# Kernel tuning notes

Hardware: AMD Instinct MI355X
Metric: run time of the kernel (lower is better)

Reference implementation:

```python
import jax, jax.numpy as jnp
import numpy as np

B, L, C, H, W = 4, 32, 16, 64, 64


def setup_inputs() -> dict:
    key = jax.random.key(0)
    k1, k2 = jax.random.split(key)
    # small flows so warps stay mostly local (realistic optical-flow magnitudes)
    flows = jax.random.normal(k1, (B, L, 2, H, W), dtype=jnp.float32) * 0.1
    images = jax.random.normal(k2, (B, L, C, H, W), dtype=jnp.float32)
    return {"flows": flows, "images": images}


def _wrap(x):
    # wrap_coord: map into [-1, 1) periodically (jnp.mod with positive divisor is non-negative)
    return jnp.mod(x + 1.0, 2.0) - 1.0


def _bilinear(images, ix, iy):
    # images: [B, K, C, H, W]; ix, iy: [B, K, H, W] pixel-space coords
    Bb, K, Cc, Hh, Ww = images.shape
    x0 = jnp.floor(ix).astype(jnp.int32)
    y0 = jnp.floor(iy).astype(jnp.int32)
    x1 = x0 + 1
    y1 = y0 + 1
    wx1 = ix - x0.astype(ix.dtype)
    wy1 = iy - y0.astype(iy.dtype)
    wx0 = 1.0 - wx1
    wy0 = 1.0 - wy1
    flat = images.reshape(Bb, K, Cc, Hh * Ww)

    def gat(xi, yi):
        valid = ((xi >= 0) & (xi < Ww) & (yi >= 0) & (yi < Hh)).astype(images.dtype)
        idx = (jnp.clip(yi, 0, Hh - 1) * Ww + jnp.clip(xi, 0, Ww - 1)).reshape(Bb, K, 1, Hh * Ww)
        v = jnp.take_along_axis(flat, idx, axis=3).reshape(Bb, K, Cc, Hh, Ww)
        return v * valid[:, :, None]  # zero padding outside image

    return ((wx0 * wy0)[:, :, None] * gat(x0, y0)
            + (wx1 * wy0)[:, :, None] * gat(x1, y0)
            + (wx0 * wy1)[:, :, None] * gat(x0, y1)
            + (wx1 * wy1)[:, :, None] * gat(x1, y1))


def _forward(flows, images):
    Bb, Ll, Cc, Hh, Ww = images.shape
    # cumulative flow, computed in fp32 then cast back (matches torch.cumsum(...).to(dtype))
    cum = jnp.cumsum(flows.astype(jnp.float32), axis=1).astype(flows.dtype)  # [B,L,2,H,W]
    bx = (jnp.arange(Ww, dtype=jnp.float32) + 0.5) * (2.0 / Ww) - 1.0
    by = (jnp.arange(Hh, dtype=jnp.float32) + 0.5) * (2.0 / Hh) - 1.0
    base_x = jnp.broadcast_to(bx[None, :], (Hh, Ww))
    base_y = jnp.broadcast_to(by[:, None], (Hh, Ww))
    # mask[t, k] = 1 iff k <= t (causal accumulation over past frames)
    mask = jnp.tril(jnp.ones((Ll, Ll), dtype=images.dtype))

    def step(carry, inp):
        cum_t, mrow = inp  # cum_t: [B,2,H,W], mrow: [L]
        rel = cum_t[:, None] - cum  # [B,L,2,H,W] = flow_t - flow_k
        gx = _wrap(base_x + rel[:, :, 0])
        gy = _wrap(base_y + rel[:, :, 1])
        ix = (gx + 1.0) * 0.5 * Ww - 0.5
        iy = (gy + 1.0) * 0.5 * Hh - 0.5
        warped = _bilinear(images, ix, iy)  # [B,L,C,H,W]
        out_t = jnp.einsum('blchw,l->bchw', warped, mrow)
        return carry, out_t

    _, ys = jax.lax.scan(step, None, (jnp.moveaxis(cum, 1, 0), mask))
    return jnp.moveaxis(ys, 0, 1)  # [B,L,C,H,W]


def reference(flows, images):
    return _forward(flows, images)
```

## Files before the change

### kernel.cpp

```cpp
#include <hip/hip_runtime.h>


constexpr int BN = 4, LN = 32, CN = 16, HWn = 4096;
constexpr int FRAME = CN * HWn;
constexpr size_t TIMG_BYTES = (size_t)BN * LN * HWn * CN * 2;
constexpr size_t CUM_BYTES  = (size_t)BN * LN * HWn * 2 * 4;

__global__ __launch_bounds__(256) void prep_timg(
        const float* __restrict__ img, float4* __restrict__ timg) {
    const int bi = blockIdx.x, tile = bi & 15, f = bi >> 4;
    const int p = (tile << 8) + threadIdx.x;
    const float* src = img + (size_t)f * FRAME + p;
#pragma unroll
    for (int g = 0; g < 2; ++g) {
        union { float4 f4; _Float16 h[8]; } cell;
#pragma unroll
        for (int j = 0; j < 8; ++j)
            cell.h[j] = (_Float16)src[(g * 8 + j) * HWn];
        timg[((size_t)f * 2 + g) * HWn + p] = cell.f4;
    }
}

__global__ __launch_bounds__(256) void prep_cum(
        const float* __restrict__ flows, float2* __restrict__ cum) {
    const int b = blockIdx.x >> 4;
    const int p = ((blockIdx.x & 15) << 8) + threadIdx.x;
    const float* fl = flows + (size_t)b * (LN * 2 * HWn) + p;
    float cx = 0.f, cy = 0.f;
    for (int l = 0; l < LN; ++l) {
        cx += fl[(2 * l) * HWn];
        cy += fl[(2 * l + 1) * HWn];
        cum[(size_t)(b * LN + l) * HWn + p] = make_float2(cx, cy);
    }
}

__device__ __forceinline__ void px_step(const float4* __restrict__ fr,
                                        float2 ct, float2 ck,
                                        float bx, float by,
                                        float* __restrict__ acc) {
    float vx = (bx + (ct.x - ck.x)) + 1.0f;
    float vy = (by + (ct.y - ck.y)) + 1.0f;
    float mx = vx - 2.0f * floorf(vx * 0.5f);
    float my = vy - 2.0f * floorf(vy * 0.5f);
    float ix = ((mx - 1.0f) + 1.0f) * 32.0f - 0.5f;
    float iy = ((my - 1.0f) + 1.0f) * 32.0f - 0.5f;
    float xf = floorf(ix), yf = floorf(iy);
    int x0 = (int)xf, y0 = (int)yf;
    float wx1 = ix - xf, wy1 = iy - yf;
    float wx0 = 1.0f - wx1, wy0 = 1.0f - wy1;
    wx0 = (x0 >= 0) ? wx0 : 0.0f;
    wx1 = (x0 <= 62) ? wx1 : 0.0f;
    wy0 = (y0 >= 0) ? wy0 : 0.0f;
    wy1 = (y0 <= 62) ? wy1 : 0.0f;
    const int x0c = max(x0, 0), y0c = max(y0, 0);
    const int x1c = min(x0 + 1, 63), y1c = min(y0 + 1, 63);
    const float w00 = wx0 * wy0, w10 = wx1 * wy0;
    const float w01 = wx0 * wy1, w11 = wx1 * wy1;
    union { float4 f4; _Float16 h[8]; } g00, g10, g01, g11;
    g00.f4 = fr[(y0c << 6) + x0c];
    g10.f4 = fr[(y0c << 6) + x1c];
    g01.f4 = fr[(y1c << 6) + x0c];
    g11.f4 = fr[(y1c << 6) + x1c];
#pragma unroll
    for (int c = 0; c < 8; ++c)
        acc[c] += ((w00 * (float)g00.h[c] + w10 * (float)g10.h[c])
                   + w01 * (float)g01.h[c]) + w11 * (float)g11.h[c];
}

__global__ __launch_bounds__(1024, 4) void gsps_lds(
        const float2* __restrict__ cum,
        const char* __restrict__ timg,
        float* __restrict__ out) {
    extern __shared__ char smem[];
    const int bid = blockIdx.x;
    const int xs  = bid & 7;
    const int b   = xs >> 1;
    const int pxh = xs & 1;
    const int seq = bid >> 3;
    const int pair = seq & 15;
    const int chh  = seq >> 4;
    const int tid = threadIdx.x;
    const int t1 = 31 - pair;
    const int t2 = pair;

    const int px0 = (pxh << 11) + tid;
    const int px1 = px0 + 1024;
    const float bx0 = ((float)(px0 & 63) + 0.5f) * 0.03125f - 1.0f;
    const float by0 = ((float)(px0 >> 6) + 0.5f) * 0.03125f - 1.0f;
    const float bx1 = ((float)(px1 & 63) + 0.5f) * 0.03125f - 1.0f;
    const float by1 = ((float)(px1 >> 6) + 0.5f) * 0.03125f - 1.0f;

    const float2* cb = cum + (size_t)b * (LN * HWn);
    const size_t chunk0 = (((size_t)b * LN * 2) + chh) << 16;
    const unsigned wbase = (unsigned)(tid & ~63) << 4;

#define STAGE(KK, BUF) do {                                                   \
    const char* gsrc = timg + chunk0 + ((size_t)(KK) << 17);                  \
    _Pragma("unroll")                                                         \
    for (int j = 0; j < 4; ++j) {                                             \
        __builtin_amdgcn_global_load_lds(                                     \
            (const __attribute__((address_space(1))) void*)                  \
                (gsrc + j * 16384 + tid * 16),                                \
            (__attribute__((address_space(3))) void*)                        \
                (smem + ((BUF) << 16) + wbase + j * 16384),                   \
            16, 0, 0);                                                        \
    }                                                                         \
} while (0)

    float acc0[8] = {0}, acc1[8] = {0};
    float2 ct0 = make_float2(0.f, 0.f), ct1 = ct0;
    float2 ckp0 = cb[px0], ckp1 = cb[px1];

    STAGE(0, 0);

    for (int i = 0; i < 33; ++i) {
        const bool ph2 = (i > t1);
        const int k = ph2 ? (i - t1 - 1) : i;
        const int t = ph2 ? t2 : t1;

        __syncthreads();
        if (i < 32) {
            const int kn = (i + 1 > t1) ? (i - t1) : (i + 1);
            STAGE(kn, (i + 1) & 1);
        }

        const float2 ck0 = ckp0, ck1 = ckp1;
        if (i < 32) {
            const int kn = (i + 1 > t1) ? (i - t1) : (i + 1);
            ckp0 = cb[kn * HWn + px0];
            ckp1 = cb[kn * HWn + px1];
        }
        if (k == 0) {
            ct0 = cb[t * HWn + px0];
            ct1 = cb[t * HWn + px1];
#pragma unroll
            for (int c = 0; c < 8; ++c) { acc0[c] = 0.f; acc1[c] = 0.f; }
        }
        const float4* fr = (const float4*)(smem + ((i & 1) << 16));
        px_step(fr, ct0, ck0, bx0, by0, acc0);
        px_step(fr, ct1, ck1, bx1, by1, acc1);

        if (k == t) {
            float* op = out + ((size_t)(b * LN + t) * CN + chh * 8) * HWn;
#pragma unroll
            for (int c = 0; c < 8; ++c) {
                op[c * HWn + px0] = acc0[c];
                op[c * HWn + px1] = acc1[c];
            }
        }
    }
#undef STAGE
}

__global__ __launch_bounds__(256) void gsps_slow(
        const float* __restrict__ flows,
        const float* __restrict__ img,
        float* __restrict__ out) {
    const int bi = blockIdx.x;
    const int tile = bi & 15;
    const int rest = bi >> 4;
    const int t = 31 - (rest & 31);
    const int b = rest >> 5;
    const int p = (tile << 8) + threadIdx.x;
    const int h = p >> 6, w = p & 63;
    const float base_x = ((float)w + 0.5f) * 0.03125f - 1.0f;
    const float base_y = ((float)h + 0.5f) * 0.03125f - 1.0f;
    const float* fl = flows + (size_t)b * (LN * 2 * HWn) + p;

    float ctx = 0.f, cty = 0.f;
    for (int j = 0; j <= t; ++j) { ctx += fl[(2*j)*HWn]; cty += fl[(2*j+1)*HWn]; }

    float acc[16];
#pragma unroll
    for (int c = 0; c < 16; ++c) acc[c] = 0.f;

    float ckx = 0.f, cky = 0.f;
    for (int k = 0; k <= t; ++k) {
        ckx += fl[(2*k)*HWn]; cky += fl[(2*k+1)*HWn];
        float vx = (base_x + (ctx - ckx)) + 1.0f;
        float vy = (base_y + (cty - cky)) + 1.0f;
        float mx = vx - 2.0f * floorf(vx * 0.5f);
        float my = vy - 2.0f * floorf(vy * 0.5f);
        const float ix = ((mx - 1.0f) + 1.0f) * 32.0f - 0.5f;
        const float iy = ((my - 1.0f) + 1.0f) * 32.0f - 0.5f;
        const float x0f = floorf(ix), y0f = floorf(iy);
        const int x0 = (int)x0f, y0 = (int)y0f;
        const float wx1 = ix - x0f, wy1 = iy - y0f;
        const float wx0 = 1.0f - wx1, wy0 = 1.0f - wy1;
        const int x1 = x0 + 1, y1 = y0 + 1;
        const float fx0 = (x0 >= 0) ? 1.0f : 0.0f;
        const float fx1 = (x1 <= 63) ? 1.0f : 0.0f;
        const float fy0 = (y0 >= 0) ? 1.0f : 0.0f;
        const float fy1 = (y1 <= 63) ? 1.0f : 0.0f;
        const int x0c = (x0 < 0) ? 0 : x0, x1c = (x1 > 63) ? 63 : x1;
        const int y0c = (y0 < 0) ? 0 : y0, y1c = (y1 > 63) ? 63 : y1;
        const float w00 = (wx0*wy0)*(fx0*fy0), w10 = (wx1*wy0)*(fx1*fy0);
        const float w01 = (wx0*wy1)*(fx0*fy1), w11 = (wx1*wy1)*(fx1*fy1);
        const float* frm = img + (size_t)(b * LN + k) * FRAME;
        const int i00 = (y0c<<6)+x0c, i10 = (y0c<<6)+x1c;
        const int i01 = (y1c<<6)+x0c, i11 = (y1c<<6)+x1c;
#pragma unroll
        for (int c = 0; c < 16; ++c) {
            const float* pl = frm + c * HWn;
            acc[c] += ((w00*pl[i00] + w10*pl[i10]) + w01*pl[i01]) + w11*pl[i11];
        }
    }
    float* op = out + (size_t)(b * LN + t) * FRAME + p;
#pragma unroll
    for (int c = 0; c < 16; ++c) op[c * HWn] = acc[c];
}

extern "C" void kernel_launch(void* const* d_in, const int* in_sizes, int n_in,
                              void* d_out, int out_size, void* d_ws, size_t ws_size,
                              hipStream_t stream) {
    const float* flows  = (const float*)d_in[0];
    const float* images = (const float*)d_in[1];
    float* out = (float*)d_out;

    bool fast = (ws_size >= TIMG_BYTES + CUM_BYTES);
    if (fast) {
        hipError_t e = hipFuncSetAttribute(
            reinterpret_cast<const void*>(&gsps_lds),
            hipFuncAttributeMaxDynamicSharedMemorySize, 131072);
        if (e != hipSuccess) fast = false;
    }
    if (fast) {
        float4* timg = (float4*)d_ws;
        float2* cumw = (float2*)((char*)d_ws + TIMG_BYTES);
        prep_timg<<<BN * LN * 16, 256, 0, stream>>>(images, timg);
        prep_cum<<<BN * 16, 256, 0, stream>>>(flows, cumw);
        gsps_lds<<<256, 1024, 131072, stream>>>(cumw, (const char*)timg, out);
    } else {
        gsps_slow<<<BN * LN * 16, 256, 0, stream>>>(flows, images, out);
    }
}
```

Measured before the change: 89.77 us.

## Single-buffer LDS stage with smaller blocks and more workgroups

```diff
diff --git a/kernel.cpp b/kernel.cpp
--- a/kernel.cpp
+++ b/kernel.cpp
@@ -42,8 +42,8 @@
     float vy = (by + (ct.y - ck.y)) + 1.0f;
     float mx = vx - 2.0f * floorf(vx * 0.5f);
     float my = vy - 2.0f * floorf(vy * 0.5f);
-    float ix = ((mx - 1.0f) + 1.0f) * 32.0f - 0.5f;
-    float iy = ((my - 1.0f) + 1.0f) * 32.0f - 0.5f;
+    float ix = mx * 32.0f - 0.5f;
+    float iy = my * 32.0f - 0.5f;
     float xf = floorf(ix), yf = floorf(iy);
     int x0 = (int)xf, y0 = (int)yf;
     float wx1 = ix - xf, wy1 = iy - yf;
@@ -57,34 +57,33 @@
     const float w00 = wx0 * wy0, w10 = wx1 * wy0;
     const float w01 = wx0 * wy1, w11 = wx1 * wy1;
     union { float4 f4; _Float16 h[8]; } g00, g10, g01, g11;
-    g00.f4 = fr[(y0c << 6) + x0c];
-    g10.f4 = fr[(y0c << 6) + x1c];
-    g01.f4 = fr[(y1c << 6) + x0c];
-    g11.f4 = fr[(y1c << 6) + x1c];
+    const int r0 = (y0c << 6), r1 = (y1c << 6);
+    g00.f4 = fr[r0 + x0c];
+    g10.f4 = fr[r0 + x1c];
+    g01.f4 = fr[r1 + x0c];
+    g11.f4 = fr[r1 + x1c];
 #pragma unroll
     for (int c = 0; c < 8; ++c)
         acc[c] += ((w00 * (float)g00.h[c] + w10 * (float)g10.h[c])
                    + w01 * (float)g01.h[c]) + w11 * (float)g11.h[c];
 }
 
-__global__ __launch_bounds__(1024, 4) void gsps_lds(
+__global__ __launch_bounds__(512, 4) void gsps_lds(
         const float2* __restrict__ cum,
         const char* __restrict__ timg,
         float* __restrict__ out) {
     extern __shared__ char smem[];
     const int bid = blockIdx.x;
-    const int xs  = bid & 7;
-    const int b   = xs >> 1;
-    const int pxh = xs & 1;
-    const int seq = bid >> 3;
-    const int pair = seq & 15;
-    const int chh  = seq >> 4;
-    const int tid = threadIdx.x;
+    const int pxq  = ((bid & 1) << 1) | ((bid >> 3) & 1);
+    const int b    = (bid >> 1) & 3;
+    const int pair = (bid >> 4) & 15;
+    const int chh  = bid >> 8;
+    const int tid  = threadIdx.x;
     const int t1 = 31 - pair;
     const int t2 = pair;
 
-    const int px0 = (pxh << 11) + tid;
-    const int px1 = px0 + 1024;
+    const int px0 = (pxq << 10) + tid;
+    const int px1 = px0 + 512;
     const float bx0 = ((float)(px0 & 63) + 0.5f) * 0.03125f - 1.0f;
     const float by0 = ((float)(px0 >> 6) + 0.5f) * 0.03125f - 1.0f;
     const float bx1 = ((float)(px1 & 63) + 0.5f) * 0.03125f - 1.0f;
@@ -94,15 +93,15 @@
     const size_t chunk0 = (((size_t)b * LN * 2) + chh) << 16;
     const unsigned wbase = (unsigned)(tid & ~63) << 4;
 
-#define STAGE(KK, BUF) do {                                                   \
+#define STAGE(KK) do {                                                        \
     const char* gsrc = timg + chunk0 + ((size_t)(KK) << 17);                  \
     _Pragma("unroll")                                                         \
-    for (int j = 0; j < 4; ++j) {                                             \
+    for (int j = 0; j < 8; ++j) {                                             \
         __builtin_amdgcn_global_load_lds(                                     \
             (const __attribute__((address_space(1))) void*)                  \
-                (gsrc + j * 16384 + tid * 16),                                \
+                (gsrc + j * 8192 + tid * 16),                                 \
             (__attribute__((address_space(3))) void*)                        \
-                (smem + ((BUF) << 16) + wbase + j * 16384),                   \
+                (smem + wbase + j * 8192),                                    \
             16, 0, 0);                                                        \
     }                                                                         \
 } while (0)
@@ -110,8 +109,6 @@
     float acc0[8] = {0}, acc1[8] = {0};
     float2 ct0 = make_float2(0.f, 0.f), ct1 = ct0;
     float2 ckp0 = cb[px0], ckp1 = cb[px1];
-
-    STAGE(0, 0);
 
     for (int i = 0; i < 33; ++i) {
         const bool ph2 = (i > t1);
@@ -119,10 +116,8 @@
         const int t = ph2 ? t2 : t1;
 
         __syncthreads();
-        if (i < 32) {
-            const int kn = (i + 1 > t1) ? (i - t1) : (i + 1);
-            STAGE(kn, (i + 1) & 1);
-        }
+        STAGE(i == 0 ? 0 : k);
+        __syncthreads();
 
         const float2 ck0 = ckp0, ck1 = ckp1;
         if (i < 32) {
@@ -136,7 +131,7 @@
 #pragma unroll
             for (int c = 0; c < 8; ++c) { acc0[c] = 0.f; acc1[c] = 0.f; }
         }
-        const float4* fr = (const float4*)(smem + ((i & 1) << 16));
+        const float4* fr = (const float4*)smem;
         px_step(fr, ct0, ck0, bx0, by0, acc0);
         px_step(fr, ct1, ck1, bx1, by1, acc1);
 
@@ -221,7 +216,7 @@
     if (fast) {
         hipError_t e = hipFuncSetAttribute(
             reinterpret_cast<const void*>(&gsps_lds),
-            hipFuncAttributeMaxDynamicSharedMemorySize, 131072);
+            hipFuncAttributeMaxDynamicSharedMemorySize, 65536);
         if (e != hipSuccess) fast = false;
     }
     if (fast) {
@@ -229,7 +224,7 @@
         float2* cumw = (float2*)((char*)d_ws + TIMG_BYTES);
         prep_timg<<<BN * LN * 16, 256, 0, stream>>>(images, timg);
         prep_cum<<<BN * 16, 256, 0, stream>>>(flows, cumw);
-        gsps_lds<<<256, 1024, 131072, stream>>>(cumw, (const char*)timg, out);
+        gsps_lds<<<512, 512, 65536, stream>>>(cumw, (const char*)timg, out);
     } else {
         gsps_slow<<<BN * LN * 16, 256, 0, stream>>>(flows, images, out);
     }
```

Result: slower. 95.12 us (+6.0%).

## Zero-pad image tiles to 66x66 to drop bilinear bounds checks

Applied to the files above, without the earlier changes.

```diff
diff --git a/kernel.cpp b/kernel.cpp
--- a/kernel.cpp
+++ b/kernel.cpp
@@ -3,21 +3,28 @@
 
 constexpr int BN = 4, LN = 32, CN = 16, HWn = 4096;
 constexpr int FRAME = CN * HWn;
-constexpr size_t TIMG_BYTES = (size_t)BN * LN * HWn * CN * 2;
+constexpr int PW = 66, PCELLS = PW * PW;
+constexpr int CHUNK_B = PCELLS * 16;
+constexpr size_t TIMG_BYTES = (size_t)BN * LN * 2 * CHUNK_B;
 constexpr size_t CUM_BYTES  = (size_t)BN * LN * HWn * 2 * 4;
 
-__global__ __launch_bounds__(256) void prep_timg(
+__global__ __launch_bounds__(1024) void prep_pad(
         const float* __restrict__ img, float4* __restrict__ timg) {
-    const int bi = blockIdx.x, tile = bi & 15, f = bi >> 4;
-    const int p = (tile << 8) + threadIdx.x;
-    const float* src = img + (size_t)f * FRAME + p;
-#pragma unroll
-    for (int g = 0; g < 2; ++g) {
+    const int f = blockIdx.x >> 1, g = blockIdx.x & 1;
+    const float* src = img + (size_t)f * FRAME + g * (8 * HWn);
+    float4* dst = timg + (size_t)blockIdx.x * PCELLS;
+    for (int q = threadIdx.x; q < PCELLS; q += 1024) {
+        const int y = q / PW, x = q - y * PW;
         union { float4 f4; _Float16 h[8]; } cell;
-#pragma unroll
-        for (int j = 0; j < 8; ++j)
-            cell.h[j] = (_Float16)src[(g * 8 + j) * HWn];
-        timg[((size_t)f * 2 + g) * HWn + p] = cell.f4;
+        if (y >= 1 && y <= 64 && x >= 1 && x <= 64) {
+            const int p = ((y - 1) << 6) + (x - 1);
+#pragma unroll
+            for (int c = 0; c < 8; ++c)
+                cell.h[c] = (_Float16)src[c * HWn + p];
+        } else {
+            cell.f4 = make_float4(0.f, 0.f, 0.f, 0.f);
+        }
+        dst[q] = cell.f4;
     }
 }
 
@@ -38,33 +45,32 @@
                                         float2 ct, float2 ck,
                                         float bx, float by,
                                         float* __restrict__ acc) {
-    float vx = (bx + (ct.x - ck.x)) + 1.0f;
-    float vy = (by + (ct.y - ck.y)) + 1.0f;
-    float mx = vx - 2.0f * floorf(vx * 0.5f);
-    float my = vy - 2.0f * floorf(vy * 0.5f);
-    float ix = ((mx - 1.0f) + 1.0f) * 32.0f - 0.5f;
-    float iy = ((my - 1.0f) + 1.0f) * 32.0f - 0.5f;
-    float xf = floorf(ix), yf = floorf(iy);
-    int x0 = (int)xf, y0 = (int)yf;
-    float wx1 = ix - xf, wy1 = iy - yf;
-    float wx0 = 1.0f - wx1, wy0 = 1.0f - wy1;
-    wx0 = (x0 >= 0) ? wx0 : 0.0f;
-    wx1 = (x0 <= 62) ? wx1 : 0.0f;
-    wy0 = (y0 >= 0) ? wy0 : 0.0f;
-    wy1 = (y0 <= 62) ? wy1 : 0.0f;
-    const int x0c = max(x0, 0), y0c = max(y0, 0);
-    const int x1c = min(x0 + 1, 63), y1c = min(y0 + 1, 63);
+    const float vx = (bx + (ct.x - ck.x)) + 1.0f;
+    const float vy = (by + (ct.y - ck.y)) + 1.0f;
+    const float ux = vx * 0.5f, uy = vy * 0.5f;
+    const float fx = ux - floorf(ux);
+    const float fy = uy - floorf(uy);
+    const float ixp = fmaf(fx, 64.0f, 0.5f);
+    const float iyp = fmaf(fy, 64.0f, 0.5f);
+    const float xf = floorf(ixp), yf = floorf(iyp);
+    const int x0p = (int)xf, y0p = (int)yf;
+    const float wx1 = ixp - xf, wy1 = iyp - yf;
+    const float wx0 = 1.0f - wx1, wy0 = 1.0f - wy1;
     const float w00 = wx0 * wy0, w10 = wx1 * wy0;
     const float w01 = wx0 * wy1, w11 = wx1 * wy1;
+    const int i00 = y0p * PW + x0p;
     union { float4 f4; _Float16 h[8]; } g00, g10, g01, g11;
-    g00.f4 = fr[(y0c << 6) + x0c];
-    g10.f4 = fr[(y0c << 6) + x1c];
-    g01.f4 = fr[(y1c << 6) + x0c];
-    g11.f4 = fr[(y1c << 6) + x1c];
-#pragma unroll
-    for (int c = 0; c < 8; ++c)
-        acc[c] += ((w00 * (float)g00.h[c] + w10 * (float)g10.h[c])
-                   + w01 * (float)g01.h[c]) + w11 * (float)g11.h[c];
+    g00.f4 = fr[i00];
+    g10.f4 = fr[i00 + 1];
+    g01.f4 = fr[i00 + PW];
+    g11.f4 = fr[i00 + PW + 1];
+#pragma unroll
+    for (int c = 0; c < 8; ++c) {
+        float s = fmaf((float)g00.h[c], w00, acc[c]);
+        s = fmaf((float)g10.h[c], w10, s);
+        s = fmaf((float)g01.h[c], w01, s);
+        acc[c] = fmaf((float)g11.h[c], w11, s);
+    }
 }
 
 __global__ __launch_bounds__(1024, 4) void gsps_lds(
@@ -79,7 +85,7 @@
     const int seq = bid >> 3;
     const int pair = seq & 15;
     const int chh  = seq >> 4;
-    const int tid = threadIdx.x;
+    const int tid  = threadIdx.x;
     const int t1 = 31 - pair;
     const int t2 = pair;
 
@@ -91,18 +97,25 @@
     const float by1 = ((float)(px1 >> 6) + 0.5f) * 0.03125f - 1.0f;
 
     const float2* cb = cum + (size_t)b * (LN * HWn);
-    const size_t chunk0 = (((size_t)b * LN * 2) + chh) << 16;
+    const size_t chunk0 = ((size_t)b * LN * 2 + chh) * CHUNK_B;
     const unsigned wbase = (unsigned)(tid & ~63) << 4;
 
 #define STAGE(KK, BUF) do {                                                   \
-    const char* gsrc = timg + chunk0 + ((size_t)(KK) << 17);                  \
+    const char* gsrc = timg + chunk0 + (size_t)(KK) * (2 * CHUNK_B);          \
+    char* lbase = smem + (BUF) * CHUNK_B + wbase;                             \
     _Pragma("unroll")                                                         \
     for (int j = 0; j < 4; ++j) {                                             \
         __builtin_amdgcn_global_load_lds(                                     \
             (const __attribute__((address_space(1))) void*)                  \
-                (gsrc + j * 16384 + tid * 16),                                \
-            (__attribute__((address_space(3))) void*)                        \
-                (smem + ((BUF) << 16) + wbase + j * 16384),                   \
+                (gsrc + (j * 16384 + tid * 16)),                              \
+            (__attribute__((address_space(3))) void*)(lbase + j * 16384),    \
+            16, 0, 0);                                                        \
+    }                                                                         \
+    if (tid < PCELLS - 4096) {                     \
+        __builtin_amdgcn_global_load_lds(                                     \
+            (const __attribute__((address_space(1))) void*)                  \
+                (gsrc + (65536 + tid * 16)),                                  \
+            (__attribute__((address_space(3))) void*)(lbase + 65536),        \
             16, 0, 0);                                                        \
     }                                                                         \
 } while (0)
@@ -136,7 +149,7 @@
 #pragma unroll
             for (int c = 0; c < 8; ++c) { acc0[c] = 0.f; acc1[c] = 0.f; }
         }
-        const float4* fr = (const float4*)(smem + ((i & 1) << 16));
+        const float4* fr = (const float4*)(smem + (i & 1) * CHUNK_B);
         px_step(fr, ct0, ck0, bx0, by0, acc0);
         px_step(fr, ct1, ck1, bx1, by1, acc1);
 
@@ -221,15 +234,16 @@
     if (fast) {
         hipError_t e = hipFuncSetAttribute(
             reinterpret_cast<const void*>(&gsps_lds),
-            hipFuncAttributeMaxDynamicSharedMemorySize, 131072);
+            hipFuncAttributeMaxDynamicSharedMemorySize, 2 * CHUNK_B);
         if (e != hipSuccess) fast = false;
     }
     if (fast) {
         float4* timg = (float4*)d_ws;
         float2* cumw = (float2*)((char*)d_ws + TIMG_BYTES);
-        prep_timg<<<BN * LN * 16, 256, 0, stream>>>(images, timg);
+        prep_pad<<<BN * LN * 2, 1024, 0, stream>>>(images, timg);
         prep_cum<<<BN * 16, 256, 0, stream>>>(flows, cumw);
-        gsps_lds<<<256, 1024, 131072, stream>>>(cumw, (const char*)timg, out);
+        gsps_lds<<<256, 1024, 2 * CHUNK_B, stream>>>(
+            cumw, (const char*)timg, out);
     } else {
         gsps_slow<<<BN * LN * 16, 256, 0, stream>>>(flows, images, out);
     }
```

New measurement: 91.44 us. About the same (+1.9%).
